# Kernel tuning notes

Measured on AMD Instinct MI355X. Metric: run time of the kernel, lower is better.

Reference implementation:

```python
import jax, jax.numpy as jnp
import numpy as np

N_NODES = 50000
N_EDGES = 1600000
IN_FEAT = 128
HEADS = 8
OUT_FEAT = 16


def setup_inputs() -> dict:
    key = jax.random.key(0)
    ks = jax.random.split(key, 8)
    feat = jax.random.normal(ks[0], (N_NODES, IN_FEAT), dtype=jnp.float32)
    src = jax.random.randint(ks[1], (N_EDGES,), 0, N_NODES, dtype=jnp.int32)
    dst = jax.random.randint(ks[2], (N_EDGES,), 0, N_NODES, dtype=jnp.int32)
    eps = jax.random.normal(ks[3], (N_EDGES, HEADS), dtype=jnp.float32)
    # small init scale keeps exp(log_scale) numerically tame
    W_fc = jax.random.normal(ks[4], (IN_FEAT, HEADS * OUT_FEAT), dtype=jnp.float32) * 0.05
    W_post = jax.random.normal(ks[5], (OUT_FEAT, 4), dtype=jnp.float32) * 0.05
    b_post = jax.random.normal(ks[6], (4,), dtype=jnp.float32) * 0.05
    bias = jax.random.normal(ks[7], (HEADS, OUT_FEAT), dtype=jnp.float32) * 0.05
    return {"feat": feat, "src": src, "dst": dst, "eps": eps,
            "W_fc": W_fc, "W_post": W_post, "b_post": b_post, "bias": bias}


def reference(feat, src, dst, eps, W_fc, W_post, b_post, bias):
    N = feat.shape[0]
    # node projection: [N, H, F]
    h = (feat @ W_fc).reshape(N, HEADS, OUT_FEAT)
    # per-node posterior params: [N, H, 4] -> loc_l, loc_r, log_scale_l, log_scale_r
    post = jnp.einsum('nhf,fk->nhk', h, W_post) + b_post
    loc_l, loc_r, lsl, lsr = post[..., 0], post[..., 1], post[..., 2], post[..., 3]
    # per-edge score via reparameterized sample: [E, H]
    loc = loc_l[src] + loc_r[dst]
    log_scale = lsl[src] + lsr[dst]
    e = loc + jnp.exp(log_scale) * eps
    # edge softmax over incoming edges of each dst node (per head)
    m = jax.lax.stop_gradient(jax.ops.segment_max(e, dst, num_segments=N))
    ex = jnp.exp(e - m[dst])
    denom = jax.ops.segment_sum(ex, dst, num_segments=N)
    a = ex / denom[dst]
    # weighted aggregation: sum over in-edges of h[src] * a
    msg = h[src] * a[:, :, None]                     # [E, H, F]
    out = jax.ops.segment_sum(msg, dst, num_segments=N)  # [N, H, F]
    out = out + bias[None]
    return out
```

## Files before the change

kernel.cpp:

```cpp
#include <hip/hip_runtime.h>
#include <hip/hip_fp16.h>

#define IN_FEAT 128
#define HEADS 8
#define OUT_FEAT 16
#define HF 128
#define BSHIFT 6
#define BNODES 64
#define NBMAX 1024
#define CHUNK 4096

__global__ __launch_bounds__(256) void bucket_hist_kernel(
    const int* __restrict__ dst, int* __restrict__ bucket_tot, int E, int nb)
{
    __shared__ int cnt[NBMAX];
    const int tid = threadIdx.x;
    for (int i = tid; i < nb; i += 256) cnt[i] = 0;
    __syncthreads();
    const int stride = gridDim.x * 256;
    for (int g = blockIdx.x * 256 + tid; g < E; g += stride)
        atomicAdd(&cnt[dst[g] >> BSHIFT], 1);
    __syncthreads();
    for (int i = tid; i < nb; i += 256) {
        int c = cnt[i];
        if (c) atomicAdd(&bucket_tot[i], c);
    }
}

__global__ __launch_bounds__(256) void bucket_scan_kernel(
    const int* __restrict__ bucket_tot, int* __restrict__ bucket_base,
    int* __restrict__ bucket_cursor, int nb, int E)
{
    __shared__ int sd[256];
    const int tid = threadIdx.x;
    int v[4]; int s = 0;
#pragma unroll
    for (int k = 0; k < 4; ++k) {
        int i = tid * 4 + k;
        v[k] = (i < nb) ? bucket_tot[i] : 0;
        s += v[k];
    }
    sd[tid] = s;
    __syncthreads();
    for (int off = 1; off < 256; off <<= 1) {
        int t = (tid >= off) ? sd[tid - off] : 0;
        __syncthreads();
        sd[tid] += t;
        __syncthreads();
    }
    int excl = sd[tid] - s;
#pragma unroll
    for (int k = 0; k < 4; ++k) {
        int i = tid * 4 + k;
        if (i < nb) { bucket_base[i] = excl; bucket_cursor[i] = excl; }
        excl += v[k];
    }
    if (tid == 0) bucket_base[nb] = E;
}

__global__ __launch_bounds__(256) void gemm_scatter_kernel(
    const float* __restrict__ feat, const float* __restrict__ W_fc,
    const float* __restrict__ W_post, const float* __restrict__ b_post,
    __half* __restrict__ hbuf, float* __restrict__ post, int N,
    const int* __restrict__ src, const int* __restrict__ dst,
    int* __restrict__ bucket_cursor, uint2* __restrict__ recs, int E, int nb,
    int SB)
{
    __shared__ float4 lds4[32 * 32];
    const int tid = threadIdx.x;

    if (blockIdx.x < SB) {
        int* cnt  = (int*)lds4;
        int* base = cnt + NBMAX;
        for (int i = tid; i < nb; i += 256) cnt[i] = 0;
        __syncthreads();
        const int e0 = blockIdx.x * CHUNK;
        const int e1 = min(e0 + CHUNK, E);
        for (int e = e0 + tid; e < e1; e += 256)
            atomicAdd(&cnt[dst[e] >> BSHIFT], 1);
        __syncthreads();
        for (int i = tid; i < nb; i += 256) {
            int c = cnt[i];
            base[i] = c ? atomicAdd(&bucket_cursor[i], c) : 0;
            cnt[i] = 0;
        }
        __syncthreads();
        for (int e = e0 + tid; e < e1; e += 256) {
            int d = dst[e];
            int b = d >> BSHIFT;
            int slot = base[b] + atomicAdd(&cnt[b], 1);
            recs[slot] = make_uint2((unsigned)e,
                                    ((unsigned)src[e] << BSHIFT) | (unsigned)(d & (BNODES - 1)));
        }
        return;
    }

    float* lds = (float*)lds4;
    const int node_base = (blockIdx.x - SB) * 32;

    const float4* f4 = (const float4*)feat;
    for (int i = tid; i < 32 * 32; i += 256) {
        int n = i >> 5, k4 = i & 31;
        int gn = node_base + n;
        float4 v = make_float4(0.f, 0.f, 0.f, 0.f);
        if (gn < N) v = f4[gn * 32 + k4];
        lds4[i] = v;
    }
    __syncthreads();

    const int cg = tid & 31, ng = tid >> 5;
    const int n0 = ng * 4;
    float acc[4][4];
#pragma unroll
    for (int i = 0; i < 4; i++) acc[i][0] = acc[i][1] = acc[i][2] = acc[i][3] = 0.f;

    const float4* W4 = (const float4*)W_fc;
#pragma unroll 4
    for (int k = 0; k < 128; ++k) {
        float4 w = W4[k * 32 + cg];
#pragma unroll
        for (int i = 0; i < 4; i++) {
            float f = lds[(n0 + i) * 128 + k];
            acc[i][0] += f * w.x; acc[i][1] += f * w.y;
            acc[i][2] += f * w.z; acc[i][3] += f * w.w;
        }
    }
    __half2* hb2 = (__half2*)hbuf;
#pragma unroll
    for (int i = 0; i < 4; i++) {
        int gn = node_base + n0 + i;
        if (gn < N) {
            union { uint2 u; __half2 h[2]; } pk;
            pk.h[0] = __floats2half2_rn(acc[i][0], acc[i][1]);
            pk.h[1] = __floats2half2_rn(acc[i][2], acc[i][3]);
            *(uint2*)&hb2[gn * 64 + cg * 2] = pk.u;
        }
    }
    __syncthreads();
#pragma unroll
    for (int i = 0; i < 4; i++)
        lds4[(n0 + i) * 32 + cg] = make_float4(acc[i][0], acc[i][1], acc[i][2], acc[i][3]);
    __syncthreads();

    {
        int n = tid >> 3, h = tid & 7;
        float p0 = b_post[0], p1 = b_post[1], p2 = b_post[2], p3 = b_post[3];
#pragma unroll
        for (int f = 0; f < 16; ++f) {
            float v = lds[n * 128 + h * 16 + f];
            p0 += v * W_post[f * 4 + 0];
            p1 += v * W_post[f * 4 + 1];
            p2 += v * W_post[f * 4 + 2];
            p3 += v * W_post[f * 4 + 3];
        }
        int gn = node_base + n;
        if (gn < N) {
            post[gn * 32 + 0 * 8 + h] = p0;
            post[gn * 32 + 1 * 8 + h] = p1;
            post[gn * 32 + 2 * 8 + h] = p2;
            post[gn * 32 + 3 * 8 + h] = p3;
        }
    }
}

__global__ __launch_bounds__(256) void bucket_csr_kernel(
    const uint2* __restrict__ recs, const int* __restrict__ bucket_base,
    int* __restrict__ offsets, uint2* __restrict__ csr, int N, int E)
{
    __shared__ int ncnt[BNODES];
    __shared__ int snc[BNODES];
    const int b = blockIdx.x, tid = threadIdx.x;
    const int node_lo = b << BSHIFT;
    const int rlo = bucket_base[b], rhi = bucket_base[b + 1];
    const int gn = node_lo + tid;

    if (tid < BNODES) ncnt[tid] = 0;
    __syncthreads();
    for (int r = rlo + tid; r < rhi; r += 256)
        atomicAdd(&ncnt[recs[r].y & (BNODES - 1u)], 1);
    __syncthreads();
    if (tid < BNODES) snc[tid] = ncnt[tid];
    __syncthreads();
    for (int off = 1; off < BNODES; off <<= 1) {
        int t = (tid < BNODES && tid >= off) ? snc[tid - off] : 0;
        __syncthreads();
        if (tid < BNODES) snc[tid] += t;
        __syncthreads();
    }
    int excl = (tid < BNODES) ? snc[tid] - ncnt[tid] : 0;
    if (tid < BNODES && gn < N) offsets[gn] = rlo + excl;
    if (b == 0 && tid == 0) offsets[N] = E;
    __syncthreads();
    if (tid < BNODES) ncnt[tid] = excl;
    __syncthreads();

    for (int r = rlo + tid; r < rhi; r += 256) {
        uint2 rec = recs[r];
        int dl = (int)(rec.y & (BNODES - 1u));
        unsigned s = rec.y >> BSHIFT;
        int slot = rlo + atomicAdd(&ncnt[dl], 1);
        csr[slot] = make_uint2(rec.x, s);
    }
}

__global__ __launch_bounds__(256) void agg_kernel(
    const uint2* __restrict__ csr, const int* __restrict__ offsets,
    const float* __restrict__ post, const float* __restrict__ eps,
    const __half* __restrict__ hbuf, const float* __restrict__ bias,
    float* __restrict__ out, int N)
{
    const int lane = threadIdx.x & 63;
    const int d = blockIdx.x * 4 + (threadIdx.x >> 6);
    if (d >= N) return;
    const int start = offsets[d];
    const int deg = offsets[d + 1] - start;
    const int j = lane >> 3, hh = lane & 7;
    const int h = j;
    const float dl  = post[d * 32 + 8 + hh];
    const float dls = post[d * 32 + 24 + hh];

    float2 acc = make_float2(0.f, 0.f);
    float dsum = 0.f;

    int c = 0;
    for (; c + 8 <= deg; c += 8) {
        uint2 rec = csr[start + c + j];
        int e = (int)rec.x, s = (int)rec.y;
        float ll = post[s * 32 + hh];
        float sl = post[s * 32 + 16 + hh];
        float ep = eps[(size_t)e * 8 + hh];
        float ex = __expf((ll + dl) + __expf(sl + dls) * ep);
#pragma unroll
        for (int jj = 0; jj < 8; ++jj) {
            float a = __shfl(ex, jj * 8 + h, 64);
            int  sj = __shfl(s, jj * 8, 64);
            float2 hv = __half22float2(((const __half2*)(hbuf + (size_t)sj * HF))[lane]);
            acc.x += a * hv.x;
            acc.y += a * hv.y;
            dsum += a;
        }
    }
    if (c < deg) {
        int jc = deg - c;
        uint2 rec = csr[start + c + min(j, jc - 1)];
        int e = (int)rec.x, s = (int)rec.y;
        float ll = post[s * 32 + hh];
        float sl = post[s * 32 + 16 + hh];
        float ep = eps[(size_t)e * 8 + hh];
        float ex = (j < jc) ? __expf((ll + dl) + __expf(sl + dls) * ep) : 0.f;
        for (int jj = 0; jj < jc; ++jj) {
            float a = __shfl(ex, jj * 8 + h, 64);
            int  sj = __shfl(s, jj * 8, 64);
            float2 hv = __half22float2(((const __half2*)(hbuf + (size_t)sj * HF))[lane]);
            acc.x += a * hv.x;
            acc.y += a * hv.y;
            dsum += a;
        }
    }

    float inv = (dsum > 0.f) ? 1.f / dsum : 0.f;
    float2 bv = ((const float2*)bias)[lane];
    float2 o = make_float2(acc.x * inv + bv.x, acc.y * inv + bv.y);
    ((float2*)out)[(size_t)d * 64 + lane] = o;
}

extern "C" void kernel_launch(void* const* d_in, const int* in_sizes, int n_in,
                              void* d_out, int out_size, void* d_ws, size_t ws_size,
                              hipStream_t stream)
{
    const float* feat   = (const float*)d_in[0];
    const int*   src    = (const int*)d_in[1];
    const int*   dst    = (const int*)d_in[2];
    const float* eps    = (const float*)d_in[3];
    const float* W_fc   = (const float*)d_in[4];
    const float* W_post = (const float*)d_in[5];
    const float* b_post = (const float*)d_in[6];
    const float* bias   = (const float*)d_in[7];
    float* out = (float*)d_out;

    const int N = in_sizes[0] / IN_FEAT;
    const int E = in_sizes[1];
    const int nb = (N + BNODES - 1) >> BSHIFT;
    const int SB = (E + CHUNK - 1) / CHUNK;
    const int GB = (N + 31) / 32;

    char* p = (char*)d_ws;
    auto alloc = [&](size_t bytes) {
        char* r = p;
        p += (bytes + 255) & ~size_t(255);
        return r;
    };
    __half* hbuf    = (__half*)alloc((size_t)N * HF * 2);
    float*  post    = (float*)alloc((size_t)N * 32 * 4);
    int*    offsets = (int*)alloc((size_t)(N + 1) * 4);
    int*    bucket_tot    = (int*)alloc((size_t)(NBMAX + 1) * 4);
    int*    bucket_base   = (int*)alloc((size_t)(NBMAX + 1) * 4);
    int*    bucket_cursor = (int*)alloc((size_t)(NBMAX + 1) * 4);
    uint2*  recs    = (uint2*)alloc((size_t)E * 8);
    uint2*  csr     = (uint2*)alloc((size_t)E * 8);

    hipMemsetAsync(bucket_tot, 0, (size_t)nb * 4, stream);

    bucket_hist_kernel<<<512, 256, 0, stream>>>(dst, bucket_tot, E, nb);
    bucket_scan_kernel<<<1, 256, 0, stream>>>(bucket_tot, bucket_base,
                                              bucket_cursor, nb, E);
    gemm_scatter_kernel<<<SB + GB, 256, 0, stream>>>(
        feat, W_fc, W_post, b_post, hbuf, post, N,
        src, dst, bucket_cursor, recs, E, nb, SB);
    bucket_csr_kernel<<<nb, 256, 0, stream>>>(recs, bucket_base, offsets, csr, N, E);
    agg_kernel<<<(N + 3) / 4, 256, 0, stream>>>(csr, offsets, post, eps, hbuf,
                                                bias, out, N);
}
```

Before: 310.8 us.

## Split posterior params into float2 src/dst arrays and software-pipeline edge loads

Per-node posterior values are stored as two interleaved float2 arrays (src-side loc/logscale and dst-side loc/logscale), so each gather reads one 8-byte value instead of two scattered floats. The aggregation loop is restructured into a single loop that prefetches CSR records two groups ahead and the posterior/eps gathers one group ahead, hiding the dependent-load latency behind the accumulation. The tail handling is folded into that loop through clamped indices and masking. In exchange it uses more registers and issues redundant clamped loads past the end of short neighbour lists.

```diff
diff --git a/kernel.cpp b/kernel.cpp
--- a/kernel.cpp
+++ b/kernel.cpp
@@ -61,7 +61,8 @@
 __global__ __launch_bounds__(256) void gemm_scatter_kernel(
     const float* __restrict__ feat, const float* __restrict__ W_fc,
     const float* __restrict__ W_post, const float* __restrict__ b_post,
-    __half* __restrict__ hbuf, float* __restrict__ post, int N,
+    __half* __restrict__ hbuf, float2* __restrict__ postE,
+    float2* __restrict__ postD, int N,
     const int* __restrict__ src, const int* __restrict__ dst,
     int* __restrict__ bucket_cursor, uint2* __restrict__ recs, int E, int nb,
     int SB)
@@ -155,10 +156,8 @@
         }
         int gn = node_base + n;
         if (gn < N) {
-            post[gn * 32 + 0 * 8 + h] = p0;
-            post[gn * 32 + 1 * 8 + h] = p1;
-            post[gn * 32 + 2 * 8 + h] = p2;
-            post[gn * 32 + 3 * 8 + h] = p3;
+            postE[gn * 8 + h] = make_float2(p0, p2);
+            postD[gn * 8 + h] = make_float2(p1, p3);
         }
     }
 }
@@ -205,7 +204,8 @@
 
 __global__ __launch_bounds__(256) void agg_kernel(
     const uint2* __restrict__ csr, const int* __restrict__ offsets,
-    const float* __restrict__ post, const float* __restrict__ eps,
+    const float2* __restrict__ postE, const float2* __restrict__ postD,
+    const float* __restrict__ eps,
     const __half* __restrict__ hbuf, const float* __restrict__ bias,
     float* __restrict__ out, int N)
 {
@@ -215,46 +215,41 @@
     const int start = offsets[d];
     const int deg = offsets[d + 1] - start;
     const int j = lane >> 3, hh = lane & 7;
-    const int h = j;
-    const float dl  = post[d * 32 + 8 + hh];
-    const float dls = post[d * 32 + 24 + hh];
+    const float2 dv = postD[(size_t)d * 8 + hh];
 
     float2 acc = make_float2(0.f, 0.f);
     float dsum = 0.f;
 
-    int c = 0;
-    for (; c + 8 <= deg; c += 8) {
-        uint2 rec = csr[start + c + j];
-        int e = (int)rec.x, s = (int)rec.y;
-        float ll = post[s * 32 + hh];
-        float sl = post[s * 32 + 16 + hh];
-        float ep = eps[(size_t)e * 8 + hh];
-        float ex = __expf((ll + dl) + __expf(sl + dls) * ep);
-#pragma unroll
-        for (int jj = 0; jj < 8; ++jj) {
-            float a = __shfl(ex, jj * 8 + h, 64);
-            int  sj = __shfl(s, jj * 8, 64);
-            float2 hv = __half22float2(((const __half2*)(hbuf + (size_t)sj * HF))[lane]);
-            acc.x += a * hv.x;
-            acc.y += a * hv.y;
-            dsum += a;
-        }
-    }
-    if (c < deg) {
-        int jc = deg - c;
-        uint2 rec = csr[start + c + min(j, jc - 1)];
-        int e = (int)rec.x, s = (int)rec.y;
-        float ll = post[s * 32 + hh];
-        float sl = post[s * 32 + 16 + hh];
-        float ep = eps[(size_t)e * 8 + hh];
-        float ex = (j < jc) ? __expf((ll + dl) + __expf(sl + dls) * ep) : 0.f;
-        for (int jj = 0; jj < jc; ++jj) {
-            float a = __shfl(ex, jj * 8 + h, 64);
-            int  sj = __shfl(s, jj * 8, 64);
-            float2 hv = __half22float2(((const __half2*)(hbuf + (size_t)sj * HF))[lane]);
-            acc.x += a * hv.x;
-            acc.y += a * hv.y;
-            dsum += a;
+    if (deg > 0) {
+        const int ngrp = (deg + 7) >> 3;
+        auto ldrec = [&](int g) -> uint2 {
+            int idx = g * 8 + j;
+            idx = (idx < deg) ? idx : (deg - 1);
+            return csr[start + idx];
+        };
+        uint2 recA = ldrec(0);
+        uint2 recB = ldrec(1);
+        float2 pvA = postE[(size_t)recA.y * 8 + hh];
+        float  epA = eps[(size_t)recA.x * 8 + hh];
+
+        for (int g = 0; g < ngrp; ++g) {
+            uint2 recC = ldrec(g + 2);
+            float2 pvB = postE[(size_t)recB.y * 8 + hh];
+            float  epB = eps[(size_t)recB.x * 8 + hh];
+
+            int jc = deg - g * 8; jc = (jc < 8) ? jc : 8;
+            float ex = (j < jc)
+                ? __expf((pvA.x + dv.x) + __expf(pvA.y + dv.y) * epA) : 0.f;
+            int sA = (int)recA.y;
+            for (int jj = 0; jj < jc; ++jj) {
+                float a = __shfl(ex, jj * 8 + j, 64);
+                int  sj = __shfl(sA, jj * 8, 64);
+                float2 hv = __half22float2(((const __half2*)(hbuf + (size_t)sj * HF))[lane]);
+                acc.x += a * hv.x;
+                acc.y += a * hv.y;
+                dsum += a;
+            }
+            recA = recB; recB = recC; pvA = pvB; epA = epB;
         }
     }
 
@@ -291,7 +286,8 @@
         return r;
     };
     __half* hbuf    = (__half*)alloc((size_t)N * HF * 2);
-    float*  post    = (float*)alloc((size_t)N * 32 * 4);
+    float2* postE   = (float2*)alloc((size_t)N * 8 * 8);
+    float2* postD   = (float2*)alloc((size_t)N * 8 * 8);
     int*    offsets = (int*)alloc((size_t)(N + 1) * 4);
     int*    bucket_tot    = (int*)alloc((size_t)(NBMAX + 1) * 4);
     int*    bucket_base   = (int*)alloc((size_t)(NBMAX + 1) * 4);
@@ -305,9 +301,9 @@
     bucket_scan_kernel<<<1, 256, 0, stream>>>(bucket_tot, bucket_base,
                                               bucket_cursor, nb, E);
     gemm_scatter_kernel<<<SB + GB, 256, 0, stream>>>(
-        feat, W_fc, W_post, b_post, hbuf, post, N,
+        feat, W_fc, W_post, b_post, hbuf, postE, postD, N,
         src, dst, bucket_cursor, recs, E, nb, SB);
     bucket_csr_kernel<<<nb, 256, 0, stream>>>(recs, bucket_base, offsets, csr, N, E);
-    agg_kernel<<<(N + 3) / 4, 256, 0, stream>>>(csr, offsets, post, eps, hbuf,
-                                                bias, out, N);
-}
+    agg_kernel<<<(N + 3) / 4, 256, 0, stream>>>(csr, offsets, postE, postD, eps,
+                                                hbuf, bias, out, N);
+}
```

After: 328.9 us. 5.8% more time.

## Split node GEMM across hist/scatter/CSR kernels, LDS-sort scatter, pack post params

Applied to the files above, without the earlier changes.

The node projection GEMM blocks are split into three slices and co-launched with the histogram, scatter and CSR-build kernels, so compute overlaps the latency-bound sorting phases. The scatter kernel now first sorts each chunk's edges by bucket in LDS using a permutation, then writes records in bucket order, making global stores more contiguous. Per-node posterior params are repacked into src-side and dst-side float2 arrays so the aggregation kernel does one 8-byte gather per node instead of two strided 4-byte loads. This adds LDS pressure to the scatter kernel, which may lower occupancy, and uses fixed slice sizes (300/800) for the split.

```diff
diff --git a/kernel.cpp b/kernel.cpp
--- a/kernel.cpp
+++ b/kernel.cpp
@@ -9,94 +9,17 @@
 #define BNODES 64
 #define NBMAX 1024
 #define CHUNK 4096
-
-__global__ __launch_bounds__(256) void bucket_hist_kernel(
-    const int* __restrict__ dst, int* __restrict__ bucket_tot, int E, int nb)
-{
-    __shared__ int cnt[NBMAX];
-    const int tid = threadIdx.x;
-    for (int i = tid; i < nb; i += 256) cnt[i] = 0;
-    __syncthreads();
-    const int stride = gridDim.x * 256;
-    for (int g = blockIdx.x * 256 + tid; g < E; g += stride)
-        atomicAdd(&cnt[dst[g] >> BSHIFT], 1);
-    __syncthreads();
-    for (int i = tid; i < nb; i += 256) {
-        int c = cnt[i];
-        if (c) atomicAdd(&bucket_tot[i], c);
-    }
-}
-
-__global__ __launch_bounds__(256) void bucket_scan_kernel(
-    const int* __restrict__ bucket_tot, int* __restrict__ bucket_base,
-    int* __restrict__ bucket_cursor, int nb, int E)
-{
-    __shared__ int sd[256];
-    const int tid = threadIdx.x;
-    int v[4]; int s = 0;
-#pragma unroll
-    for (int k = 0; k < 4; ++k) {
-        int i = tid * 4 + k;
-        v[k] = (i < nb) ? bucket_tot[i] : 0;
-        s += v[k];
-    }
-    sd[tid] = s;
-    __syncthreads();
-    for (int off = 1; off < 256; off <<= 1) {
-        int t = (tid >= off) ? sd[tid - off] : 0;
-        __syncthreads();
-        sd[tid] += t;
-        __syncthreads();
-    }
-    int excl = sd[tid] - s;
-#pragma unroll
-    for (int k = 0; k < 4; ++k) {
-        int i = tid * 4 + k;
-        if (i < nb) { bucket_base[i] = excl; bucket_cursor[i] = excl; }
-        excl += v[k];
-    }
-    if (tid == 0) bucket_base[nb] = E;
-}
-
-__global__ __launch_bounds__(256) void gemm_scatter_kernel(
+#define HB 512
+
+__device__ __forceinline__ void gemm_body(
     const float* __restrict__ feat, const float* __restrict__ W_fc,
     const float* __restrict__ W_post, const float* __restrict__ b_post,
-    __half* __restrict__ hbuf, float* __restrict__ post, int N,
-    const int* __restrict__ src, const int* __restrict__ dst,
-    int* __restrict__ bucket_cursor, uint2* __restrict__ recs, int E, int nb,
-    int SB)
-{
-    __shared__ float4 lds4[32 * 32];
-    const int tid = threadIdx.x;
-
-    if (blockIdx.x < SB) {
-        int* cnt  = (int*)lds4;
-        int* base = cnt + NBMAX;
-        for (int i = tid; i < nb; i += 256) cnt[i] = 0;
-        __syncthreads();
-        const int e0 = blockIdx.x * CHUNK;
-        const int e1 = min(e0 + CHUNK, E);
-        for (int e = e0 + tid; e < e1; e += 256)
-            atomicAdd(&cnt[dst[e] >> BSHIFT], 1);
-        __syncthreads();
-        for (int i = tid; i < nb; i += 256) {
-            int c = cnt[i];
-            base[i] = c ? atomicAdd(&bucket_cursor[i], c) : 0;
-            cnt[i] = 0;
-        }
-        __syncthreads();
-        for (int e = e0 + tid; e < e1; e += 256) {
-            int d = dst[e];
-            int b = d >> BSHIFT;
-            int slot = base[b] + atomicAdd(&cnt[b], 1);
-            recs[slot] = make_uint2((unsigned)e,
-                                    ((unsigned)src[e] << BSHIFT) | (unsigned)(d & (BNODES - 1)));
-        }
-        return;
-    }
-
+    __half* __restrict__ hbuf, float2* __restrict__ postE,
+    float2* __restrict__ postD, int N, int node_base, void* ldsraw)
+{
+    float4* lds4 = (float4*)ldsraw;
     float* lds = (float*)lds4;
-    const int node_base = (blockIdx.x - SB) * 32;
+    const int tid = threadIdx.x;
 
     const float4* f4 = (const float4*)feat;
     for (int i = tid; i < 32 * 32; i += 256) {
@@ -155,57 +78,208 @@
         }
         int gn = node_base + n;
         if (gn < N) {
-            post[gn * 32 + 0 * 8 + h] = p0;
-            post[gn * 32 + 1 * 8 + h] = p1;
-            post[gn * 32 + 2 * 8 + h] = p2;
-            post[gn * 32 + 3 * 8 + h] = p3;
-        }
-    }
-}
-
-__global__ __launch_bounds__(256) void bucket_csr_kernel(
+            postE[gn * 8 + h] = make_float2(p0, p2);
+            postD[gn * 8 + h] = make_float2(p1, p3);
+        }
+    }
+}
+
+__global__ __launch_bounds__(256) void hist_gemm_kernel(
+    const int* __restrict__ dst, int* __restrict__ bucket_tot, int E, int nb,
+    const float* __restrict__ feat, const float* __restrict__ W_fc,
+    const float* __restrict__ W_post, const float* __restrict__ b_post,
+    __half* __restrict__ hbuf, float2* __restrict__ postE,
+    float2* __restrict__ postD, int N, int nbase0)
+{
+    __shared__ union { int cnt[NBMAX]; float4 g[32 * 32]; } u;
+    const int tid = threadIdx.x;
+
+    if (blockIdx.x < HB) {
+        for (int i = tid; i < nb; i += 256) u.cnt[i] = 0;
+        __syncthreads();
+        const int stride = HB * 256;
+        for (int g = blockIdx.x * 256 + tid; g < E; g += stride)
+            atomicAdd(&u.cnt[dst[g] >> BSHIFT], 1);
+        __syncthreads();
+        for (int i = tid; i < nb; i += 256) {
+            int c = u.cnt[i];
+            if (c) atomicAdd(&bucket_tot[i], c);
+        }
+        return;
+    }
+    gemm_body(feat, W_fc, W_post, b_post, hbuf, postE, postD, N,
+              nbase0 + (int)(blockIdx.x - HB) * 32, (void*)u.g);
+}
+
+__global__ __launch_bounds__(256) void bucket_scan_kernel(
+    const int* __restrict__ bucket_tot, int* __restrict__ bucket_base,
+    int* __restrict__ bucket_cursor, int nb, int E)
+{
+    __shared__ int sd[256];
+    const int tid = threadIdx.x;
+    int v[4]; int s = 0;
+#pragma unroll
+    for (int k = 0; k < 4; ++k) {
+        int i = tid * 4 + k;
+        v[k] = (i < nb) ? bucket_tot[i] : 0;
+        s += v[k];
+    }
+    sd[tid] = s;
+    __syncthreads();
+    for (int off = 1; off < 256; off <<= 1) {
+        int t = (tid >= off) ? sd[tid - off] : 0;
+        __syncthreads();
+        sd[tid] += t;
+        __syncthreads();
+    }
+    int excl = sd[tid] - s;
+#pragma unroll
+    for (int k = 0; k < 4; ++k) {
+        int i = tid * 4 + k;
+        if (i < nb) { bucket_base[i] = excl; bucket_cursor[i] = excl; }
+        excl += v[k];
+    }
+    if (tid == 0) bucket_base[nb] = E;
+}
+
+struct ScatLDS {
+    int cnt[NBMAX];
+    int base_[NBMAX];
+    int loff[NBMAX];
+    int cur[NBMAX];
+    unsigned short perm[CHUNK];
+    int sd[256];
+};
+
+__global__ __launch_bounds__(256) void scatter_gemm_kernel(
+    const int* __restrict__ src, const int* __restrict__ dst,
+    int* __restrict__ bucket_cursor, uint2* __restrict__ recs, int E, int nb,
+    int SB,
+    const float* __restrict__ feat, const float* __restrict__ W_fc,
+    const float* __restrict__ W_post, const float* __restrict__ b_post,
+    __half* __restrict__ hbuf, float2* __restrict__ postE,
+    float2* __restrict__ postD, int N, int nbase0)
+{
+    __shared__ union { ScatLDS s; float4 g[32 * 32]; } u;
+    const int tid = threadIdx.x;
+
+    if (blockIdx.x < SB) {
+        const int e0 = blockIdx.x * CHUNK;
+        const int e1 = min(e0 + CHUNK, E);
+        const int Tc = e1 - e0;
+
+        for (int i = tid; i < nb; i += 256) u.s.cnt[i] = 0;
+        __syncthreads();
+        for (int e = e0 + tid; e < e1; e += 256)
+            atomicAdd(&u.s.cnt[dst[e] >> BSHIFT], 1);
+        __syncthreads();
+
+        {
+            int v[4]; int s = 0;
+#pragma unroll
+            for (int k = 0; k < 4; ++k) {
+                int i = tid * 4 + k;
+                v[k] = (i < nb) ? u.s.cnt[i] : 0;
+                s += v[k];
+            }
+            u.s.sd[tid] = s;
+            __syncthreads();
+            for (int off = 1; off < 256; off <<= 1) {
+                int t = (tid >= off) ? u.s.sd[tid - off] : 0;
+                __syncthreads();
+                u.s.sd[tid] += t;
+                __syncthreads();
+            }
+            int excl = u.s.sd[tid] - s;
+#pragma unroll
+            for (int k = 0; k < 4; ++k) {
+                int i = tid * 4 + k;
+                if (i < nb) {
+                    u.s.loff[i] = excl;
+                    u.s.cur[i] = excl;
+                    u.s.base_[i] = v[k] ? atomicAdd(&bucket_cursor[i], v[k]) : 0;
+                }
+                excl += v[k];
+            }
+        }
+        __syncthreads();
+
+        for (int e = e0 + tid; e < e1; e += 256) {
+            int b = dst[e] >> BSHIFT;
+            int sl = atomicAdd(&u.s.cur[b], 1);
+            u.s.perm[sl] = (unsigned short)(e - e0);
+        }
+        __syncthreads();
+
+        for (int i = tid; i < Tc; i += 256) {
+            int e = e0 + (int)u.s.perm[i];
+            int d = dst[e];
+            int b = d >> BSHIFT;
+            int slot = u.s.base_[b] + (i - u.s.loff[b]);
+            recs[slot] = make_uint2((unsigned)e,
+                                    ((unsigned)src[e] << BSHIFT) | (unsigned)(d & (BNODES - 1)));
+        }
+        return;
+    }
+    gemm_body(feat, W_fc, W_post, b_post, hbuf, postE, postD, N,
+              nbase0 + (int)(blockIdx.x - SB) * 32, (void*)u.g);
+}
+
+__global__ __launch_bounds__(256) void csr_gemm_kernel(
     const uint2* __restrict__ recs, const int* __restrict__ bucket_base,
-    int* __restrict__ offsets, uint2* __restrict__ csr, int N, int E)
-{
-    __shared__ int ncnt[BNODES];
-    __shared__ int snc[BNODES];
-    const int b = blockIdx.x, tid = threadIdx.x;
-    const int node_lo = b << BSHIFT;
-    const int rlo = bucket_base[b], rhi = bucket_base[b + 1];
-    const int gn = node_lo + tid;
-
-    if (tid < BNODES) ncnt[tid] = 0;
-    __syncthreads();
-    for (int r = rlo + tid; r < rhi; r += 256)
-        atomicAdd(&ncnt[recs[r].y & (BNODES - 1u)], 1);
-    __syncthreads();
-    if (tid < BNODES) snc[tid] = ncnt[tid];
-    __syncthreads();
-    for (int off = 1; off < BNODES; off <<= 1) {
-        int t = (tid < BNODES && tid >= off) ? snc[tid - off] : 0;
-        __syncthreads();
-        if (tid < BNODES) snc[tid] += t;
-        __syncthreads();
-    }
-    int excl = (tid < BNODES) ? snc[tid] - ncnt[tid] : 0;
-    if (tid < BNODES && gn < N) offsets[gn] = rlo + excl;
-    if (b == 0 && tid == 0) offsets[N] = E;
-    __syncthreads();
-    if (tid < BNODES) ncnt[tid] = excl;
-    __syncthreads();
-
-    for (int r = rlo + tid; r < rhi; r += 256) {
-        uint2 rec = recs[r];
-        int dl = (int)(rec.y & (BNODES - 1u));
-        unsigned s = rec.y >> BSHIFT;
-        int slot = rlo + atomicAdd(&ncnt[dl], 1);
-        csr[slot] = make_uint2(rec.x, s);
-    }
+    int* __restrict__ offsets, uint2* __restrict__ csr, int N, int E, int nb,
+    const float* __restrict__ feat, const float* __restrict__ W_fc,
+    const float* __restrict__ W_post, const float* __restrict__ b_post,
+    __half* __restrict__ hbuf, float2* __restrict__ postE,
+    float2* __restrict__ postD, int nbase0)
+{
+    __shared__ union { struct { int ncnt[BNODES]; int snc[BNODES]; } c;
+                       float4 g[32 * 32]; } u;
+    const int tid = threadIdx.x;
+
+    if (blockIdx.x < (unsigned)nb) {
+        const int b = blockIdx.x;
+        const int node_lo = b << BSHIFT;
+        const int rlo = bucket_base[b], rhi = bucket_base[b + 1];
+        const int gn = node_lo + tid;
+
+        if (tid < BNODES) u.c.ncnt[tid] = 0;
+        __syncthreads();
+        for (int r = rlo + tid; r < rhi; r += 256)
+            atomicAdd(&u.c.ncnt[recs[r].y & (BNODES - 1u)], 1);
+        __syncthreads();
+        if (tid < BNODES) u.c.snc[tid] = u.c.ncnt[tid];
+        __syncthreads();
+        for (int off = 1; off < BNODES; off <<= 1) {
+            int t = (tid < BNODES && tid >= off) ? u.c.snc[tid - off] : 0;
+            __syncthreads();
+            if (tid < BNODES) u.c.snc[tid] += t;
+            __syncthreads();
+        }
+        int excl = (tid < BNODES) ? u.c.snc[tid] - u.c.ncnt[tid] : 0;
+        if (tid < BNODES && gn < N) offsets[gn] = rlo + excl;
+        if (b == 0 && tid == 0) offsets[N] = E;
+        __syncthreads();
+        if (tid < BNODES) u.c.ncnt[tid] = excl;
+        __syncthreads();
+
+        for (int r = rlo + tid; r < rhi; r += 256) {
+            uint2 rec = recs[r];
+            int dl = (int)(rec.y & (BNODES - 1u));
+            unsigned s = rec.y >> BSHIFT;
+            int slot = rlo + atomicAdd(&u.c.ncnt[dl], 1);
+            csr[slot] = make_uint2(rec.x, s);
+        }
+        return;
+    }
+    gemm_body(feat, W_fc, W_post, b_post, hbuf, postE, postD, N,
+              nbase0 + (int)(blockIdx.x - nb) * 32, (void*)u.g);
 }
 
 __global__ __launch_bounds__(256) void agg_kernel(
     const uint2* __restrict__ csr, const int* __restrict__ offsets,
-    const float* __restrict__ post, const float* __restrict__ eps,
+    const float2* __restrict__ postE, const float2* __restrict__ postD,
+    const float* __restrict__ eps,
     const __half* __restrict__ hbuf, const float* __restrict__ bias,
     float* __restrict__ out, int N)
 {
@@ -215,9 +289,7 @@
     const int start = offsets[d];
     const int deg = offsets[d + 1] - start;
     const int j = lane >> 3, hh = lane & 7;
-    const int h = j;
-    const float dl  = post[d * 32 + 8 + hh];
-    const float dls = post[d * 32 + 24 + hh];
+    const float2 dv = postD[(size_t)d * 8 + hh];
 
     float2 acc = make_float2(0.f, 0.f);
     float dsum = 0.f;
@@ -226,13 +298,12 @@
     for (; c + 8 <= deg; c += 8) {
         uint2 rec = csr[start + c + j];
         int e = (int)rec.x, s = (int)rec.y;
-        float ll = post[s * 32 + hh];
-        float sl = post[s * 32 + 16 + hh];
+        float2 pv = postE[(size_t)s * 8 + hh];
         float ep = eps[(size_t)e * 8 + hh];
-        float ex = __expf((ll + dl) + __expf(sl + dls) * ep);
+        float ex = __expf((pv.x + dv.x) + __expf(pv.y + dv.y) * ep);
 #pragma unroll
         for (int jj = 0; jj < 8; ++jj) {
-            float a = __shfl(ex, jj * 8 + h, 64);
+            float a = __shfl(ex, jj * 8 + j, 64);
             int  sj = __shfl(s, jj * 8, 64);
             float2 hv = __half22float2(((const __half2*)(hbuf + (size_t)sj * HF))[lane]);
             acc.x += a * hv.x;
@@ -244,12 +315,11 @@
         int jc = deg - c;
         uint2 rec = csr[start + c + min(j, jc - 1)];
         int e = (int)rec.x, s = (int)rec.y;
-        float ll = post[s * 32 + hh];
-        float sl = post[s * 32 + 16 + hh];
+        float2 pv = postE[(size_t)s * 8 + hh];
         float ep = eps[(size_t)e * 8 + hh];
-        float ex = (j < jc) ? __expf((ll + dl) + __expf(sl + dls) * ep) : 0.f;
+        float ex = (j < jc) ? __expf((pv.x + dv.x) + __expf(pv.y + dv.y) * ep) : 0.f;
         for (int jj = 0; jj < jc; ++jj) {
-            float a = __shfl(ex, jj * 8 + h, 64);
+            float a = __shfl(ex, jj * 8 + j, 64);
             int  sj = __shfl(s, jj * 8, 64);
             float2 hv = __half22float2(((const __half2*)(hbuf + (size_t)sj * HF))[lane]);
             acc.x += a * hv.x;
@@ -284,6 +354,10 @@
     const int SB = (E + CHUNK - 1) / CHUNK;
     const int GB = (N + 31) / 32;
 
+    int GA = 300; if (GA > GB) GA = GB;
+    int GBB = 800; if (GA + GBB > GB) GBB = GB - GA;
+    int GC = GB - GA - GBB;
+
     char* p = (char*)d_ws;
     auto alloc = [&](size_t bytes) {
         char* r = p;
@@ -291,7 +365,8 @@
         return r;
     };
     __half* hbuf    = (__half*)alloc((size_t)N * HF * 2);
-    float*  post    = (float*)alloc((size_t)N * 32 * 4);
+    float2* postE   = (float2*)alloc((size_t)N * 8 * 8);
+    float2* postD   = (float2*)alloc((size_t)N * 8 * 8);
     int*    offsets = (int*)alloc((size_t)(N + 1) * 4);
     int*    bucket_tot    = (int*)alloc((size_t)(NBMAX + 1) * 4);
     int*    bucket_base   = (int*)alloc((size_t)(NBMAX + 1) * 4);
@@ -301,13 +376,17 @@
 
     hipMemsetAsync(bucket_tot, 0, (size_t)nb * 4, stream);
 
-    bucket_hist_kernel<<<512, 256, 0, stream>>>(dst, bucket_tot, E, nb);
+    hist_gemm_kernel<<<HB + GA, 256, 0, stream>>>(
+        dst, bucket_tot, E, nb,
+        feat, W_fc, W_post, b_post, hbuf, postE, postD, N, 0);
     bucket_scan_kernel<<<1, 256, 0, stream>>>(bucket_tot, bucket_base,
                                               bucket_cursor, nb, E);
-    gemm_scatter_kernel<<<SB + GB, 256, 0, stream>>>(
-        feat, W_fc, W_post, b_post, hbuf, post, N,
-        src, dst, bucket_cursor, recs, E, nb, SB);
-    bucket_csr_kernel<<<nb, 256, 0, stream>>>(recs, bucket_base, offsets, csr, N, E);
-    agg_kernel<<<(N + 3) / 4, 256, 0, stream>>>(csr, offsets, post, eps, hbuf,
-                                                bias, out, N);
-}
+    scatter_gemm_kernel<<<SB + GBB, 256, 0, stream>>>(
+        src, dst, bucket_cursor, recs, E, nb, SB,
+        feat, W_fc, W_post, b_post, hbuf, postE, postD, N, GA * 32);
+    csr_gemm_kernel<<<nb + GC, 256, 0, stream>>>(
+        recs, bucket_base, offsets, csr, N, E, nb,
+        feat, W_fc, W_post, b_post, hbuf, postE, postD, (GA + GBB) * 32);
+    agg_kernel<<<(N + 3) / 4, 256, 0, stream>>>(csr, offsets, postE, postD, eps,
+                                                hbuf, bias, out, N);
+}
```

Result: slower. 320.3 us (+3.1%).
